# Optimization experiments

Hardware: AMD Instinct MI355X
Metric: run time of the kernel (lower is better)

## Reference

```python
import jax, jax.numpy as jnp
import numpy as np
import math

D = 768
H = 8
DK = D // H
FF = 1024
EPS = 1e-5


def _layer_norm(x, g, b):
    m = jnp.mean(x, axis=-1, keepdims=True)
    v = jnp.mean((x - m) ** 2, axis=-1, keepdims=True)
    return (x - m) * jax.lax.rsqrt(v + EPS) * g + b


def _mha(x, attention_mask, Wq, bq, Wv, bv, g, b):
    # x: (B,S,D); attention_mask: (B,S,1) bool (True = masked/padding query row)
    B, S, _ = x.shape
    q = (x @ Wq + bq).reshape(B, S, H, DK).transpose(0, 2, 1, 3)  # (B,H,S,dk)
    # NOTE: original code uses the V projection for BOTH k and v (k = self.V(x))
    kv = (x @ Wv + bv).reshape(B, S, H, DK).transpose(0, 2, 1, 3)
    k = kv
    v = kv
    w = jnp.einsum('bhqd,bhkd->bhqk', q, k) / math.sqrt(DK)  # (B,H,S,S)
    pad = attention_mask[:, None, :, :]                      # (B,1,S,1) -> bcast (B,1,S,S)
    causal = jnp.triu(jnp.ones((S, S), dtype=bool), k=1)     # look-ahead mask
    mask = pad | causal
    w = jnp.where(mask, jnp.float32(-1e9), w)
    # NOTE: original uses nn.Softmax(dim=2) -> softmax over the QUERY axis
    score = jax.nn.softmax(w, axis=2)
    o = jnp.einsum('bhqk,bhkd->bhqd', score, v)              # (B,H,S,dk)
    o = o.transpose(0, 2, 1, 3).reshape(B, S, D)
    return _layer_norm(o + x, g, b)


def _ffn(x, W1, b1, W2, b2, g, b):
    h = jax.nn.relu(x @ W1 + b1)
    return _layer_norm(h @ W2 + b2 + x, g, b)


def setup_inputs() -> dict:
    key = jax.random.key(0)
    ks = jax.random.split(key, 16)
    B, S = 8, 1024
    sc = 0.02
    inp = {
        'x': jax.random.normal(ks[0], (B, S, D), dtype=jnp.float32),
        'attention_mask': jax.random.randint(ks[1], (B, S, 1), 0, 2).astype(bool),
    }
    for i, pre in enumerate(['a1', 'a2']):
        inp[pre + '_Wq'] = jax.random.normal(ks[2 + 4 * i], (D, D), dtype=jnp.float32) * sc
        inp[pre + '_bq'] = jnp.zeros((D,), dtype=jnp.float32)
        inp[pre + '_Wv'] = jax.random.normal(ks[3 + 4 * i], (D, D), dtype=jnp.float32) * sc
        inp[pre + '_bv'] = jnp.zeros((D,), dtype=jnp.float32)
        inp[pre + '_g'] = jnp.ones((D,), dtype=jnp.float32)
        inp[pre + '_b'] = jnp.zeros((D,), dtype=jnp.float32)
    inp['f_W1'] = jax.random.normal(ks[10], (D, FF), dtype=jnp.float32) * sc
    inp['f_b1'] = jnp.zeros((FF,), dtype=jnp.float32)
    inp['f_W2'] = jax.random.normal(ks[11], (FF, D), dtype=jnp.float32) * sc
    inp['f_b2'] = jnp.zeros((D,), dtype=jnp.float32)
    inp['f_g'] = jnp.ones((D,), dtype=jnp.float32)
    inp['f_b'] = jnp.zeros((D,), dtype=jnp.float32)
    return inp


def reference(x, attention_mask,
              a1_Wq, a1_bq, a1_Wv, a1_bv, a1_g, a1_b,
              a2_Wq, a2_bq, a2_Wv, a2_bv, a2_g, a2_b,
              f_W1, f_b1, f_W2, f_b2, f_g, f_b):
    x = _mha(x, attention_mask, a1_Wq, a1_bq, a1_Wv, a1_bv, a1_g, a1_b)
    x = _mha(x, attention_mask, a2_Wq, a2_bq, a2_Wv, a2_bv, a2_g, a2_b)
    x = _ffn(x, f_W1, f_b1, f_W2, f_b2, f_g, f_b)
    return x
```

## Files before the change

### kernel.cpp

```cpp
#include <hip/hip_runtime.h>
#include <cstddef>

#define BB 8
#define SS 1024
#define DD 768
#define HH 8
#define DKK 96
#define FFF 1024
#define MM (BB*SS)
#define QVW 1536
#define SM_SCALE 0.10206207261596577f
#define NT2 8

typedef unsigned short ushort_t;
typedef short short8 __attribute__((ext_vector_type(8)));
typedef float f32x4 __attribute__((ext_vector_type(4)));
typedef ushort_t us4 __attribute__((ext_vector_type(4)));

__device__ __forceinline__ ushort_t f2b(float f) {
    union { float f; unsigned u; } x; x.f = f;
    unsigned r = x.u + 0x7fffu + ((x.u >> 16) & 1u);
    return (ushort_t)(r >> 16);
}
__device__ __forceinline__ float b2f(ushort_t u) {
    union { unsigned u; float f; } x; x.u = ((unsigned)u) << 16;
    return x.f;
}
__device__ __forceinline__ void gload16(const ushort_t* g, void* lds_base) {
    __builtin_amdgcn_global_load_lds(
        (const __attribute__((address_space(1))) unsigned int*)g,
        (__attribute__((address_space(3))) unsigned int*)lds_base, 16, 0, 0);
}

__global__ __launch_bounds__(256) void castWT(
    const float* __restrict__ W, ushort_t* __restrict__ Wt, int K, int N)
{
    __shared__ float T[32][33];
    const int tx = threadIdx.x & 31, ty = threadIdx.x >> 5;
    const int n0 = blockIdx.x * 32, k0 = blockIdx.y * 32;
    #pragma unroll
    for (int r = 0; r < 4; ++r)
        T[ty + 8*r][tx] = W[(size_t)(k0 + ty + 8*r) * N + n0 + tx];
    __syncthreads();
    #pragma unroll
    for (int r = 0; r < 4; ++r)
        Wt[(size_t)(n0 + ty + 8*r) * K + k0 + tx] = f2b(T[tx][ty + 8*r]);
}

__global__ __launch_bounds__(256) void castWT4(
    const float* __restrict__ Wa, const float* __restrict__ Wb,
    const float* __restrict__ Wc, const float* __restrict__ Wd,
    ushort_t* __restrict__ Ta, ushort_t* __restrict__ Tb,
    ushort_t* __restrict__ Tc, ushort_t* __restrict__ Td)
{
    __shared__ float T[32][33];
    const float* W; ushort_t* Wt;
    switch (blockIdx.z) {
        case 0:  W = Wa; Wt = Ta; break;
        case 1:  W = Wb; Wt = Tb; break;
        case 2:  W = Wc; Wt = Tc; break;
        default: W = Wd; Wt = Td; break;
    }
    const int tx = threadIdx.x & 31, ty = threadIdx.x >> 5;
    const int n0 = blockIdx.x * 32, k0 = blockIdx.y * 32;
    #pragma unroll
    for (int r = 0; r < 4; ++r)
        T[ty + 8*r][tx] = W[(size_t)(k0 + ty + 8*r) * DD + n0 + tx];
    __syncthreads();
    #pragma unroll
    for (int r = 0; r < 4; ++r)
        Wt[(size_t)(n0 + ty + 8*r) * DD + k0 + tx] = f2b(T[tx][ty + 8*r]);
}

__global__ __launch_bounds__(256) void cast_f2b(
    const float* __restrict__ in, ushort_t* __restrict__ out, int n4)
{
    const int i = blockIdx.x * 256 + threadIdx.x;
    if (i >= n4) return;
    const float4 v = ((const float4*)in)[i];
    us4 o; o.x = f2b(v.x); o.y = f2b(v.y); o.z = f2b(v.z); o.w = f2b(v.w);
    ((us4*)out)[i] = o;
}

template<int RELU>
__global__ __launch_bounds__(256) void gemm_bt(
    const ushort_t* __restrict__ A, const ushort_t* __restrict__ Bt,
    const float* __restrict__ bias, const float* __restrict__ bias2, int bN,
    ushort_t* __restrict__ C, int K, int N)
{
    __shared__ ushort_t S[128*136];
    ushort_t* As = S;
    ushort_t* Bs = S + 128*64;
    const int tid  = threadIdx.x;
    const int lane = tid & 63, wave = tid >> 6;
    const int wm = wave >> 1, wn = wave & 1;
    const int n = lane & 15, quad = lane >> 4;
    const int sx = n & 7;
    const int bm = blockIdx.y * 128, bn = blockIdx.x * 128;

    f32x4 acc[4][4];
    #pragma unroll
    for (int i = 0; i < 4; ++i)
        #pragma unroll
        for (int j = 0; j < 4; ++j) acc[i][j] = (f32x4){0.f, 0.f, 0.f, 0.f};

    for (int k0 = 0; k0 < K; k0 += 64) {
        #pragma unroll
        for (int it = 0; it < 4; ++it) {
            const int u   = (it*4 + wave)*64 + lane;
            const int row = u >> 3;
            const int c   = (u & 7) ^ (row & 7);
            gload16(A  + (size_t)(bm + row) * K + k0 + c*8, (char*)As + (it*4 + wave)*1024);
            gload16(Bt + (size_t)(bn + row) * K + k0 + c*8, (char*)Bs + (it*4 + wave)*1024);
        }
        __syncthreads();
        #pragma unroll
        for (int ks = 0; ks < 2; ++ks) {
            short8 af[4], bf[4];
            #pragma unroll
            for (int i = 0; i < 4; ++i)
                af[i] = *(short8*)&As[((wm*64 + i*16 + n)*8 + ((ks*4 + quad) ^ sx))*8];
            #pragma unroll
            for (int j = 0; j < 4; ++j)
                bf[j] = *(short8*)&Bs[((wn*64 + j*16 + n)*8 + ((ks*4 + quad) ^ sx))*8];
            #pragma unroll
            for (int i = 0; i < 4; ++i)
                #pragma unroll
                for (int j = 0; j < 4; ++j)
                    acc[i][j] = __builtin_amdgcn_mfma_f32_16x16x32_bf16(af[i], bf[j], acc[i][j], 0, 0, 0);
        }
        __syncthreads();
    }
    #pragma unroll
    for (int j = 0; j < 4; ++j) {
        const int col = wn*64 + j*16 + n;
        const int gcol = bn + col;
        const float bsv = (gcol < bN) ? bias[gcol] : bias2[gcol - bN];
        #pragma unroll
        for (int i = 0; i < 4; ++i) {
            const int lrow = wm*64 + i*16 + quad*4;
            #pragma unroll
            for (int r = 0; r < 4; ++r) {
                float v = acc[i][j][r] + bsv;
                if (RELU) v = fmaxf(v, 0.f);
                S[(lrow + r)*136 + col] = f2b(v);
            }
        }
    }
    __syncthreads();
    #pragma unroll
    for (int it = 0; it < 8; ++it) {
        const int u = it*256 + tid;
        const int grow = u >> 4, gc = u & 15;
        *(short8*)(C + (size_t)(bm + grow)*N + bn + gc*8) = *(short8*)&S[grow*136 + gc*8];
    }
}

__global__ __launch_bounds__(512) void attn_sums(
    const ushort_t* __restrict__ QV, const int* __restrict__ amask,
    float* __restrict__ lpart)
{
    __shared__ ushort_t Qs[128*128];
    __shared__ ushort_t Ks[2][64*128];
    __shared__ float colsum[2][8][64];
    const int tid = threadIdx.x, lane = tid & 63, wave = tid >> 6;
    const int n = lane & 15, quad = lane >> 4, sx = n & 7;
    const int hwid = blockIdx.x;
    const int v = (hwid & 7) * 32 + (hwid >> 3);
    const int px = v & 3, h = (v >> 2) & 7, b = v >> 5;
    const ushort_t* Qh = QV + (size_t)b*SS*QVW + h*DKK;
    const ushort_t* Kh = QV + (size_t)b*SS*QVW + DD + h*DKK;
    float* lpq = lpart + (size_t)(b*HH + h)*NT2*SS;

    #pragma unroll
    for (int half = 0; half < 2; ++half) {
        const int qt2 = half ? (7 - px) : px;
        const int q0 = qt2 * 128;
        const int ktmax = 2*qt2 + 1;
        #pragma unroll
        for (int it = 0; it < 4; ++it) {
            const int u = (it*8 + wave)*64 + lane;
            const int row = u >> 4, c = (u & 15) ^ (row & 7);
            if (c < 12)
                gload16(Qh + (size_t)(q0 + row)*QVW + c*8, (char*)Qs + (it*8 + wave)*1024);
        }
        const int4 mv = *(const int4*)&amask[b*SS + q0 + wave*16 + quad*4];
        const int mr[4] = {mv.x, mv.y, mv.z, mv.w};
        #pragma unroll
        for (int it = 0; it < 2; ++it) {
            const int u = (it*8 + wave)*64 + lane;
            const int row = u >> 4, c = (u & 15) ^ (row & 7);
            if (c < 12)
                gload16(Kh + (size_t)row*QVW + c*8, (char*)Ks[0] + (it*8 + wave)*1024);
        }
        __syncthreads();
        short8 aq[3];
        #pragma unroll
        for (int ks = 0; ks < 3; ++ks)
            aq[ks] = *(short8*)&Qs[((wave*16 + n)*16 + ((ks*4 + quad) ^ sx))*8];

        int cur = 0;
        for (int kt = 0; kt <= ktmax; ++kt) {
            const int k0 = kt * 64;
            if (kt < ktmax) {
                #pragma unroll
                for (int it = 0; it < 2; ++it) {
                    const int u = (it*8 + wave)*64 + lane;
                    const int row = u >> 4, c = (u & 15) ^ (row & 7);
                    if (c < 12)
                        gload16(Kh + (size_t)(k0 + 64 + row)*QVW + c*8,
                                (char*)Ks[cur^1] + (it*8 + wave)*1024);
                }
            }
            if (kt > 0 && tid < 64) {
                const float s = colsum[cur^1][0][tid] + colsum[cur^1][1][tid]
                              + colsum[cur^1][2][tid] + colsum[cur^1][3][tid]
                              + colsum[cur^1][4][tid] + colsum[cur^1][5][tid]
                              + colsum[cur^1][6][tid] + colsum[cur^1][7][tid];
                lpq[(size_t)qt2*SS + (k0 - 64) + tid] = s;
            }
            #pragma unroll
            for (int ns = 0; ns < 4; ++ns) {
                f32x4 sa = (f32x4){0.f, 0.f, 0.f, 0.f};
                #pragma unroll
                for (int ks = 0; ks < 3; ++ks) {
                    const short8 bk = *(short8*)&Ks[cur][((ns*16 + n)*16 + ((ks*4 + quad) ^ sx))*8];
                    sa = __builtin_amdgcn_mfma_f32_16x16x32_bf16(aq[ks], bk, sa, 0, 0, 0);
                }
                const int kl = ns*16 + n;
                const int keyg = k0 + kl;
                float s = 0.f;
                #pragma unroll
                for (int r = 0; r < 4; ++r) {
                    const int qg = q0 + wave*16 + quad*4 + r;
                    const bool dead = (mr[r] != 0) || (keyg > qg);
                    s += dead ? 0.f : __expf(sa[r] * SM_SCALE);
                }
                s += __shfl_xor(s, 16);
                s += __shfl_xor(s, 32);
                if (quad == 0) colsum[cur][wave][kl] = s;
            }
            __syncthreads();
            cur ^= 1;
        }
        if (tid < 64) {
            const int pb = ktmax & 1;
            const float s = colsum[pb][0][tid] + colsum[pb][1][tid]
                          + colsum[pb][2][tid] + colsum[pb][3][tid]
                          + colsum[pb][4][tid] + colsum[pb][5][tid]
                          + colsum[pb][6][tid] + colsum[pb][7][tid];
            lpq[(size_t)qt2*SS + ktmax*64 + tid] = s;
        }
    }
}

__global__ __launch_bounds__(256) void transpose_scale(
    const ushort_t* __restrict__ QV, const float* __restrict__ lpart,
    ushort_t* __restrict__ Vt)
{
    __shared__ ushort_t T[64][104];
    __shared__ float rlv[64];
    const int tid = threadIdx.x;
    const int k0 = blockIdx.x * 64, h = blockIdx.y, b = blockIdx.z;
    const ushort_t* src = QV + (size_t)b*SS*QVW + DD + h*DKK;
    for (int s = tid; s < 768; s += 256) {
        const int r = s / 12, c = s % 12;
        *(short8*)&T[r][c*8] = *(const short8*)(src + (size_t)(k0 + r)*QVW + c*8);
    }
    if (tid < 64) {
        const float* lp = lpart + (size_t)(b*HH + h)*NT2*SS;
        float l = 0.f;
        for (int qt2 = k0 >> 7; qt2 < NT2; ++qt2) l += lp[(size_t)qt2*SS + k0 + tid];
        rlv[tid] = (l > 0.f) ? (1.f / l) : 0.f;
    }
    __syncthreads();
    ushort_t* dst = Vt + ((size_t)b*HH + h)*DKK*SS;
    for (int s = tid; s < 768; s += 256) {
        const int dk = s >> 3, c = s & 7;
        short8 v;
        #pragma unroll
        for (int i = 0; i < 8; ++i)
            v[i] = (short)f2b(b2f(T[c*8 + i][dk]) * rlv[c*8 + i]);
        *(short8*)(dst + (size_t)dk*SS + k0 + c*8) = v;
    }
}

__global__ __launch_bounds__(512) void attn_pv_re(
    const ushort_t* __restrict__ QV, const int* __restrict__ amask,
    const ushort_t* __restrict__ Vt, ushort_t* __restrict__ O)
{
    __shared__ ushort_t Qs[128*128];
    __shared__ ushort_t Ks[2][64*128];
    __shared__ ushort_t Vs[2][96*64];
    __shared__ ushort_t Es[128*64];
    const int tid = threadIdx.x, lane = tid & 63, wave = tid >> 6;
    const int n = lane & 15, quad = lane >> 4, sx = n & 7;
    const int hwid = blockIdx.x;
    const int v = (hwid & 7) * 32 + (hwid >> 3);
    const int px = v & 3, h = (v >> 2) & 7, b = v >> 5;
    const ushort_t* Qh = QV + (size_t)b*SS*QVW + h*DKK;
    const ushort_t* Kh = QV + (size_t)b*SS*QVW + DD + h*DKK;
    const ushort_t* Vth = Vt + ((size_t)b*HH + h)*DKK*SS;

    #pragma unroll
    for (int half = 0; half < 2; ++half) {
        const int qt2 = half ? (7 - px) : px;
        const int q0 = qt2 * 128;
        const int ktmax = 2*qt2 + 1;
        #pragma unroll
        for (int it = 0; it < 4; ++it) {
            const int u = (it*8 + wave)*64 + lane;
            const int row = u >> 4, c = (u & 15) ^ (row & 7);
            if (c < 12)
                gload16(Qh + (size_t)(q0 + row)*QVW + c*8, (char*)Qs + (it*8 + wave)*1024);
        }
        const int4 mv = *(const int4*)&amask[b*SS + q0 + wave*16 + quad*4];
        const int mr[4] = {mv.x, mv.y, mv.z, mv.w};
        #pragma unroll
        for (int it = 0; it < 2; ++it) {
            const int u = (it*8 + wave)*64 + lane;
            const int row = u >> 4, c = (u & 15) ^ (row & 7);
            if (c < 12)
                gload16(Kh + (size_t)row*QVW + c*8, (char*)Ks[0] + (it*8 + wave)*1024);
        }
        #pragma unroll
        for (int it = 0; it < 2; ++it) {
            if (it*8 + wave < 12) {
                const int u = (it*8 + wave)*64 + lane;
                const int row = u >> 3, c = (u & 7) ^ (row & 7);
                gload16(Vth + (size_t)row*SS + c*8, (char*)Vs[0] + (it*8 + wave)*1024);
            }
        }
        __syncthreads();
        short8 aq[3];
        #pragma unroll
        for (int ks = 0; ks < 3; ++ks)
            aq[ks] = *(short8*)&Qs[((wave*16 + n)*16 + ((ks*4 + quad) ^ sx))*8];

        f32x4 acc[6];
        #pragma unroll
        for (int t = 0; t < 6; ++t) acc[t] = (f32x4){0.f, 0.f, 0.f, 0.f};

        int cur = 0;
        for (int kt = 0; kt <= ktmax; ++kt) {
            const int k0 = kt * 64;
            if (kt < ktmax) {
                #pragma unroll
                for (int it = 0; it < 2; ++it) {
                    const int u = (it*8 + wave)*64 + lane;
                    const int row = u >> 4, c = (u & 15) ^ (row & 7);
                    if (c < 12)
                        gload16(Kh + (size_t)(k0 + 64 + row)*QVW + c*8,
                                (char*)Ks[cur^1] + (it*8 + wave)*1024);
                }
                #pragma unroll
                for (int it = 0; it < 2; ++it) {
                    if (it*8 + wave < 12) {
                        const int u = (it*8 + wave)*64 + lane;
                        const int row = u >> 3, c = (u & 7) ^ (row & 7);
                        gload16(Vth + (size_t)row*SS + k0 + 64 + c*8,
                                (char*)Vs[cur^1] + (it*8 + wave)*1024);
                    }
                }
            }
            #pragma unroll
            for (int ns = 0; ns < 4; ++ns) {
                f32x4 sa = (f32x4){0.f, 0.f, 0.f, 0.f};
                #pragma unroll
                for (int ks = 0; ks < 3; ++ks) {
                    const short8 bk = *(short8*)&Ks[cur][((ns*16 + n)*16 + ((ks*4 + quad) ^ sx))*8];
                    sa = __builtin_amdgcn_mfma_f32_16x16x32_bf16(aq[ks], bk, sa, 0, 0, 0);
                }
                const int kl = ns*16 + n;
                const int keyg = k0 + kl;
                #pragma unroll
                for (int r = 0; r < 4; ++r) {
                    const int lq = quad*4 + r;
                    const int trow = wave*16 + lq;
                    const bool dead = (mr[r] != 0) || (keyg > q0 + trow);
                    const float e = dead ? 0.f : __expf(sa[r] * SM_SCALE);
                    Es[trow*64 + (((kl >> 3) ^ (lq & 7)) * 8) + (kl & 7)] = f2b(e);
                }
            }
            asm volatile("s_waitcnt lgkmcnt(0)" ::: "memory");
            __builtin_amdgcn_sched_barrier(0);

            #pragma unroll
            for (int kk = 0; kk < 2; ++kk) {
                const short8 ae = *(short8*)&Es[((wave*16 + n)*8 + ((kk*4 + quad) ^ sx))*8];
                #pragma unroll
                for (int nt = 0; nt < 6; ++nt) {
                    const short8 bv = *(short8*)&Vs[cur][((nt*16 + n)*8 + ((kk*4 + quad) ^ sx))*8];
                    acc[nt] = __builtin_amdgcn_mfma_f32_16x16x32_bf16(ae, bv, acc[nt], 0, 0, 0);
                }
            }
            __syncthreads();
            cur ^= 1;
        }
        #pragma unroll
        for (int nt = 0; nt < 6; ++nt) {
            #pragma unroll
            for (int r = 0; r < 4; ++r) {
                const int q = q0 + wave*16 + quad*4 + r;
                O[((size_t)b*SS + q)*DD + h*DKK + nt*16 + n] = f2b(acc[nt][r]);
            }
        }
    }
}

__device__ __forceinline__ float block_sum256(float s, float* tmp4)
{
    #pragma unroll
    for (int off = 32; off > 0; off >>= 1) s += __shfl_down(s, off);
    __syncthreads();
    if ((threadIdx.x & 63) == 0) tmp4[threadIdx.x >> 6] = s;
    __syncthreads();
    return tmp4[0] + tmp4[1] + tmp4[2] + tmp4[3];
}

template<int XBF, int RBF, int OUTF32>
__global__ __launch_bounds__(256) void resid_ln(
    const void* __restrict__ X, const void* __restrict__ R,
    const float* __restrict__ g, const float* __restrict__ beta,
    ushort_t* __restrict__ OutB, float* __restrict__ OutF)
{
    __shared__ float tmp4[4];
    const int row = blockIdx.x;
    const int tid = threadIdx.x;
    float v[3], s = 0.f;
    #pragma unroll
    for (int i = 0; i < 3; ++i) {
        const size_t idx = (size_t)row * DD + tid + 256*i;
        const float xv = XBF ? b2f(((const ushort_t*)X)[idx]) : ((const float*)X)[idx];
        const float rv = RBF ? b2f(((const ushort_t*)R)[idx]) : ((const float*)R)[idx];
        v[i] = xv + rv;
        s += v[i];
    }
    const float mu = block_sum256(s, tmp4) * (1.f / DD);
    float qv = 0.f;
    #pragma unroll
    for (int i = 0; i < 3; ++i) { const float d = v[i] - mu; qv += d * d; }
    const float inv = rsqrtf(block_sum256(qv, tmp4) * (1.f / DD) + 1e-5f);
    #pragma unroll
    for (int i = 0; i < 3; ++i) {
        const int c = tid + 256*i;
        const float o = (v[i] - mu) * inv * g[c] + beta[c];
        if (OUTF32) OutF[(size_t)row * DD + c] = o;
        else        OutB[(size_t)row * DD + c] = f2b(o);
    }
}

extern "C" void kernel_launch(void* const* d_in, const int* in_sizes, int n_in,
                              void* d_out, int out_size, void* d_ws, size_t ws_size,
                              hipStream_t stream)
{
    (void)in_sizes; (void)n_in; (void)out_size; (void)ws_size;
    const float* x0    = (const float*)d_in[0];
    const int*   amask = (const int*)d_in[1];
    const float* a1_Wq = (const float*)d_in[2];
    const float* a1_bq = (const float*)d_in[3];
    const float* a1_Wv = (const float*)d_in[4];
    const float* a1_bv = (const float*)d_in[5];
    const float* a1_g  = (const float*)d_in[6];
    const float* a1_b  = (const float*)d_in[7];
    const float* a2_Wq = (const float*)d_in[8];
    const float* a2_bq = (const float*)d_in[9];
    const float* a2_Wv = (const float*)d_in[10];
    const float* a2_bv = (const float*)d_in[11];
    const float* a2_g  = (const float*)d_in[12];
    const float* a2_b  = (const float*)d_in[13];
    const float* f_W1  = (const float*)d_in[14];
    const float* f_b1  = (const float*)d_in[15];
    const float* f_W2  = (const float*)d_in[16];
    const float* f_b2  = (const float*)d_in[17];
    const float* f_g   = (const float*)d_in[18];
    const float* f_b   = (const float*)d_in[19];

    char* ws = (char*)d_ws;
    size_t off = 0;
    auto alloc = [&](size_t bytes) { void* p = ws + off; off += (bytes + 255) & ~(size_t)255; return p; };
    ushort_t* WqvT1 = (ushort_t*)alloc((size_t)QVW*DD*2);
    ushort_t* WqvT2 = (ushort_t*)alloc((size_t)QVW*DD*2);
    ushort_t* W1T   = (ushort_t*)alloc((size_t)DD*FFF*2);
    ushort_t* W2T   = (ushort_t*)alloc((size_t)DD*FFF*2);
    ushort_t* xb0   = (ushort_t*)alloc((size_t)MM*DD*2);
    ushort_t* xb1   = (ushort_t*)alloc((size_t)MM*DD*2);
    ushort_t* xb2   = (ushort_t*)alloc((size_t)MM*DD*2);
    ushort_t* Ob    = (ushort_t*)alloc((size_t)MM*DD*2);
    ushort_t* QVb   = (ushort_t*)alloc((size_t)MM*QVW*2);
    ushort_t* hb    = QVb;
    ushort_t* Vtb   = (ushort_t*)alloc((size_t)MM*DD*2);
    float* lpart = (float*)alloc((size_t)BB*HH*NT2*SS*4);
    float* out = (float*)d_out;

    const dim3 blk(256);
    const dim3 blk512(512);
    const dim3 gat(256);
    const dim3 gtr(SS/64, HH, BB);
    const dim3 gqv(QVW/128, MM/128);
    const dim3 gf1(FFF/128, MM/128);
    const dim3 gf2(DD/128, MM/128);

    castWT4<<<dim3(DD/32, DD/32, 4), blk, 0, stream>>>(
        a1_Wq, a1_Wv, a2_Wq, a2_Wv,
        WqvT1, WqvT1 + (size_t)DD*DD, WqvT2, WqvT2 + (size_t)DD*DD);
    castWT<<<dim3(FFF/32, DD/32), blk, 0, stream>>>(f_W1, W1T, DD, FFF);
    castWT<<<dim3(DD/32, FFF/32), blk, 0, stream>>>(f_W2, W2T, FFF, DD);
    cast_f2b<<<(MM*DD/4 + 255)/256, blk, 0, stream>>>(x0, xb0, MM*DD/4);

    gemm_bt<0><<<gqv, blk, 0, stream>>>(xb0, WqvT1, a1_bq, a1_bv, DD, QVb, DD, QVW);
    attn_sums<<<gat, blk512, 0, stream>>>(QVb, amask, lpart);
    transpose_scale<<<gtr, blk, 0, stream>>>(QVb, lpart, Vtb);
    attn_pv_re<<<gat, blk512, 0, stream>>>(QVb, amask, Vtb, Ob);
    resid_ln<1,0,0><<<dim3(MM), blk, 0, stream>>>(Ob, x0, a1_g, a1_b, xb1, nullptr);

    gemm_bt<0><<<gqv, blk, 0, stream>>>(xb1, WqvT2, a2_bq, a2_bv, DD, QVb, DD, QVW);
    attn_sums<<<gat, blk512, 0, stream>>>(QVb, amask, lpart);
    transpose_scale<<<gtr, blk, 0, stream>>>(QVb, lpart, Vtb);
    attn_pv_re<<<gat, blk512, 0, stream>>>(QVb, amask, Vtb, Ob);
    resid_ln<1,1,0><<<dim3(MM), blk, 0, stream>>>(Ob, xb1, a2_g, a2_b, xb2, nullptr);

    gemm_bt<1><<<gf1, blk, 0, stream>>>(xb2, W1T, f_b1, f_b1, FFF, hb, DD, FFF);
    gemm_bt<0><<<gf2, blk, 0, stream>>>(hb, W2T, f_b2, f_b2, DD, Ob, FFF, DD);
    resid_ln<1,1,1><<<dim3(MM), blk, 0, stream>>>(Ob, xb2, f_g, f_b, nullptr, out);
}
```

Before: 387.9 us.

## Rewrite attention PV kernel with 32x32 MFMA and register-resident probabilities

Result: slower. 409.0 us (+5.4%).

```diff
diff --git a/kernel.cpp b/kernel.cpp
--- a/kernel.cpp
+++ b/kernel.cpp
@@ -15,7 +15,9 @@
 typedef unsigned short ushort_t;
 typedef short short8 __attribute__((ext_vector_type(8)));
 typedef float f32x4 __attribute__((ext_vector_type(4)));
+typedef float f32x16 __attribute__((ext_vector_type(16)));
 typedef ushort_t us4 __attribute__((ext_vector_type(4)));
+typedef unsigned uint2v __attribute__((ext_vector_type(2)));
 
 __device__ __forceinline__ ushort_t f2b(float f) {
     union { float f; unsigned u; } x; x.f = f;
@@ -30,6 +32,14 @@
     __builtin_amdgcn_global_load_lds(
         (const __attribute__((address_space(1))) unsigned int*)g,
         (__attribute__((address_space(3))) unsigned int*)lds_base, 16, 0, 0);
+}
+__device__ __forceinline__ void plswap(unsigned& a, unsigned& b) {
+#if __has_builtin(__builtin_amdgcn_permlane32_swap)
+    uint2v r = __builtin_amdgcn_permlane32_swap(a, b, false, false);
+    a = r[0]; b = r[1];
+#else
+    asm("v_permlane32_swap_b32 %0, %1" : "+v"(a), "+v"(b));
+#endif
 }
 
 __global__ __launch_bounds__(256) void castWT(
@@ -285,16 +295,14 @@
     }
 }
 
-__global__ __launch_bounds__(512) void attn_pv_re(
+__global__ __launch_bounds__(256, 2) void attn_pv_re(
     const ushort_t* __restrict__ QV, const int* __restrict__ amask,
     const ushort_t* __restrict__ Vt, ushort_t* __restrict__ O)
 {
-    __shared__ ushort_t Qs[128*128];
     __shared__ ushort_t Ks[2][64*128];
     __shared__ ushort_t Vs[2][96*64];
-    __shared__ ushort_t Es[128*64];
     const int tid = threadIdx.x, lane = tid & 63, wave = tid >> 6;
-    const int n = lane & 15, quad = lane >> 4, sx = n & 7;
+    const int ln31 = lane & 31, hi = lane >> 5;
     const int hwid = blockIdx.x;
     const int v = (hwid & 7) * 32 + (hwid >> 3);
     const int px = v & 3, h = (v >> 2) & 7, b = v >> 5;
@@ -307,102 +315,104 @@
         const int qt2 = half ? (7 - px) : px;
         const int q0 = qt2 * 128;
         const int ktmax = 2*qt2 + 1;
+        const int qrow = q0 + wave*32 + ln31;
+        short8 bq[6];
+        #pragma unroll
+        for (int t = 0; t < 6; ++t)
+            bq[t] = *(const short8*)(Qh + (size_t)qrow*QVW + t*16 + hi*8);
+        const bool padq = amask[b*SS + qrow] != 0;
+
         #pragma unroll
         for (int it = 0; it < 4; ++it) {
-            const int u = (it*8 + wave)*64 + lane;
+            const int u = (it*4 + wave)*64 + lane;
             const int row = u >> 4, c = (u & 15) ^ (row & 7);
             if (c < 12)
-                gload16(Qh + (size_t)(q0 + row)*QVW + c*8, (char*)Qs + (it*8 + wave)*1024);
-        }
-        const int4 mv = *(const int4*)&amask[b*SS + q0 + wave*16 + quad*4];
-        const int mr[4] = {mv.x, mv.y, mv.z, mv.w};
-        #pragma unroll
-        for (int it = 0; it < 2; ++it) {
-            const int u = (it*8 + wave)*64 + lane;
-            const int row = u >> 4, c = (u & 15) ^ (row & 7);
-            if (c < 12)
-                gload16(Kh + (size_t)row*QVW + c*8, (char*)Ks[0] + (it*8 + wave)*1024);
-        }
-        #pragma unroll
-        for (int it = 0; it < 2; ++it) {
-            if (it*8 + wave < 12) {
-                const int u = (it*8 + wave)*64 + lane;
-                const int row = u >> 3, c = (u & 7) ^ (row & 7);
-                gload16(Vth + (size_t)row*SS + c*8, (char*)Vs[0] + (it*8 + wave)*1024);
-            }
+                gload16(Kh + (size_t)row*QVW + c*8, (char*)Ks[0] + (it*4 + wave)*1024);
+        }
+        #pragma unroll
+        for (int it = 0; it < 3; ++it) {
+            const int u = (it*4 + wave)*64 + lane;
+            const int row = u >> 3, c = (u & 7) ^ (row & 7);
+            gload16(Vth + (size_t)row*SS + c*8, (char*)Vs[0] + (it*4 + wave)*1024);
         }
         __syncthreads();
-        short8 aq[3];
-        #pragma unroll
-        for (int ks = 0; ks < 3; ++ks)
-            aq[ks] = *(short8*)&Qs[((wave*16 + n)*16 + ((ks*4 + quad) ^ sx))*8];
-
-        f32x4 acc[6];
-        #pragma unroll
-        for (int t = 0; t < 6; ++t) acc[t] = (f32x4){0.f, 0.f, 0.f, 0.f};
+
+        f32x16 acc[3];
+        #pragma unroll
+        for (int db = 0; db < 3; ++db)
+            #pragma unroll
+            for (int i = 0; i < 16; ++i) acc[db][i] = 0.f;
 
         int cur = 0;
         for (int kt = 0; kt <= ktmax; ++kt) {
             const int k0 = kt * 64;
             if (kt < ktmax) {
                 #pragma unroll
-                for (int it = 0; it < 2; ++it) {
-                    const int u = (it*8 + wave)*64 + lane;
+                for (int it = 0; it < 4; ++it) {
+                    const int u = (it*4 + wave)*64 + lane;
                     const int row = u >> 4, c = (u & 15) ^ (row & 7);
                     if (c < 12)
                         gload16(Kh + (size_t)(k0 + 64 + row)*QVW + c*8,
-                                (char*)Ks[cur^1] + (it*8 + wave)*1024);
-                }
-                #pragma unroll
-                for (int it = 0; it < 2; ++it) {
-                    if (it*8 + wave < 12) {
-                        const int u = (it*8 + wave)*64 + lane;
-                        const int row = u >> 3, c = (u & 7) ^ (row & 7);
-                        gload16(Vth + (size_t)row*SS + k0 + 64 + c*8,
-                                (char*)Vs[cur^1] + (it*8 + wave)*1024);
+                                (char*)Ks[cur^1] + (it*4 + wave)*1024);
+                }
+                #pragma unroll
+                for (int it = 0; it < 3; ++it) {
+                    const int u = (it*4 + wave)*64 + lane;
+                    const int row = u >> 3, c = (u & 7) ^ (row & 7);
+                    gload16(Vth + (size_t)row*SS + k0 + 64 + c*8,
+                            (char*)Vs[cur^1] + (it*4 + wave)*1024);
+                }
+            }
+            #pragma unroll
+            for (int kb = 0; kb < 2; ++kb) {
+                f32x16 sk;
+                #pragma unroll
+                for (int i = 0; i < 16; ++i) sk[i] = 0.f;
+                const int krow = kb*32 + ln31;
+                #pragma unroll
+                for (int t = 0; t < 6; ++t) {
+                    const short8 ak = *(short8*)&Ks[cur][krow*128 + (((t*2 + hi) ^ (krow & 7))*8)];
+                    sk = __builtin_amdgcn_mfma_f32_32x32x16_bf16(ak, bq[t], sk, 0, 0, 0);
+                }
+                const int kbase = k0 + kb*32 + 4*hi;
+                float p[16];
+                #pragma unroll
+                for (int r = 0; r < 16; ++r) {
+                    const int kg = kbase + (r & 3) + 8*(r >> 2);
+                    const bool dead = padq || (kg > qrow);
+                    p[r] = dead ? 0.f : __expf(sk[r] * SM_SCALE);
+                }
+                unsigned w[8];
+                #pragma unroll
+                for (int i = 0; i < 8; ++i)
+                    asm("v_cvt_pk_bf16_f32 %0, %1, %2" : "=v"(w[i]) : "v"(p[2*i]), "v"(p[2*i+1]));
+                plswap(w[0], w[2]);
+                plswap(w[1], w[3]);
+                plswap(w[4], w[6]);
+                plswap(w[5], w[7]);
+                #pragma unroll
+                for (int s = 0; s < 2; ++s) {
+                    short8 ae;
+                    unsigned* aeu = (unsigned*)&ae;
+                    aeu[0] = w[s*4 + 0]; aeu[1] = w[s*4 + 1];
+                    aeu[2] = w[s*4 + 2]; aeu[3] = w[s*4 + 3];
+                    #pragma unroll
+                    for (int db = 0; db < 3; ++db) {
+                        const int drow = db*32 + ln31;
+                        const short8 bv = *(short8*)&Vs[cur][drow*64 + (((kb*4 + s*2 + hi) ^ (drow & 7))*8)];
+                        acc[db] = __builtin_amdgcn_mfma_f32_32x32x16_bf16(ae, bv, acc[db], 0, 0, 0);
                     }
-                }
-            }
-            #pragma unroll
-            for (int ns = 0; ns < 4; ++ns) {
-                f32x4 sa = (f32x4){0.f, 0.f, 0.f, 0.f};
-                #pragma unroll
-                for (int ks = 0; ks < 3; ++ks) {
-                    const short8 bk = *(short8*)&Ks[cur][((ns*16 + n)*16 + ((ks*4 + quad) ^ sx))*8];
-                    sa = __builtin_amdgcn_mfma_f32_16x16x32_bf16(aq[ks], bk, sa, 0, 0, 0);
-                }
-                const int kl = ns*16 + n;
-                const int keyg = k0 + kl;
-                #pragma unroll
-                for (int r = 0; r < 4; ++r) {
-                    const int lq = quad*4 + r;
-                    const int trow = wave*16 + lq;
-                    const bool dead = (mr[r] != 0) || (keyg > q0 + trow);
-                    const float e = dead ? 0.f : __expf(sa[r] * SM_SCALE);
-                    Es[trow*64 + (((kl >> 3) ^ (lq & 7)) * 8) + (kl & 7)] = f2b(e);
-                }
-            }
-            asm volatile("s_waitcnt lgkmcnt(0)" ::: "memory");
-            __builtin_amdgcn_sched_barrier(0);
-
-            #pragma unroll
-            for (int kk = 0; kk < 2; ++kk) {
-                const short8 ae = *(short8*)&Es[((wave*16 + n)*8 + ((kk*4 + quad) ^ sx))*8];
-                #pragma unroll
-                for (int nt = 0; nt < 6; ++nt) {
-                    const short8 bv = *(short8*)&Vs[cur][((nt*16 + n)*8 + ((kk*4 + quad) ^ sx))*8];
-                    acc[nt] = __builtin_amdgcn_mfma_f32_16x16x32_bf16(ae, bv, acc[nt], 0, 0, 0);
                 }
             }
             __syncthreads();
             cur ^= 1;
         }
         #pragma unroll
-        for (int nt = 0; nt < 6; ++nt) {
-            #pragma unroll
-            for (int r = 0; r < 4; ++r) {
-                const int q = q0 + wave*16 + quad*4 + r;
-                O[((size_t)b*SS + q)*DD + h*DKK + nt*16 + n] = f2b(acc[nt][r]);
+        for (int db = 0; db < 3; ++db) {
+            #pragma unroll
+            for (int r = 0; r < 16; ++r) {
+                const int q = q0 + wave*32 + (r & 3) + 8*(r >> 2) + 4*hi;
+                O[((size_t)b*SS + q)*DD + h*DKK + db*32 + ln31] = f2b(acc[db][r]);
             }
         }
     }
@@ -511,13 +521,13 @@
     gemm_bt<0><<<gqv, blk, 0, stream>>>(xb0, WqvT1, a1_bq, a1_bv, DD, QVb, DD, QVW);
     attn_sums<<<gat, blk512, 0, stream>>>(QVb, amask, lpart);
     transpose_scale<<<gtr, blk, 0, stream>>>(QVb, lpart, Vtb);
-    attn_pv_re<<<gat, blk512, 0, stream>>>(QVb, amask, Vtb, Ob);
+    attn_pv_re<<<gat, blk, 0, stream>>>(QVb, amask, Vtb, Ob);
     resid_ln<1,0,0><<<dim3(MM), blk, 0, stream>>>(Ob, x0, a1_g, a1_b, xb1, nullptr);
 
     gemm_bt<0><<<gqv, blk, 0, stream>>>(xb1, WqvT2, a2_bq, a2_bv, DD, QVb, DD, QVW);
     attn_sums<<<gat, blk512, 0, stream>>>(QVb, amask, lpart);
     transpose_scale<<<gtr, blk, 0, stream>>>(QVb, lpart, Vtb);
-    attn_pv_re<<<gat, blk512, 0, stream>>>(QVb, amask, Vtb, Ob);
+    attn_pv_re<<<gat, blk, 0, stream>>>(QVb, amask, Vtb, Ob);
     resid_ln<1,1,0><<<dim3(MM), blk, 0, stream>>>(Ob, xb1, a2_g, a2_b, xb2, nullptr);
 
     gemm_bt<1><<<gf1, blk, 0, stream>>>(xb2, W1T, f_b1, f_b1, FFF, hb, DD, FFF);
```
